# Kernel optimization log

Measured on AMD Instinct MI355X. Metric: run time of the kernel, lower is better.

## Reference

```python
import jax, jax.numpy as jnp
import numpy as np

D = 128        # dim
S = 64         # seq_len
NSYM = 128     # symbols
STACK = 16     # stack_size
DEPTH = 8      # max_depth (ACT recursion)
THRESH = 0.99  # act_threshold
EPS = 1e-6
RES = 0.1      # residual_weight
LAM_E = 0.01   # lambda_energy
TEMP = 1.0
B = 512


def _clin(xr, xi, Wr, Wi):
    # ComplexLinear: (Wr + i Wi)(xr + i xi)
    return xr @ Wr.T - xi @ Wi.T, xr @ Wi.T + xi @ Wr.T


def _cattn(zr, zi, wr, wi):
    # ComplexAttention: complex QKV projections, real softmax over concat(real,imag)
    qr, qi = _clin(zr, zi, wr[0], wi[0])
    kr, ki = _clin(zr, zi, wr[1], wi[1])
    vr, vi = _clin(zr, zi, wr[2], wi[2])
    qf = jnp.concatenate([qr, qi], -1)
    kf = jnp.concatenate([kr, ki], -1)
    a = jax.nn.softmax(jnp.einsum('bsd,btd->bst', qf, kf) * (D ** -0.5), axis=-1)
    return jnp.einsum('bst,btd->bsd', a, vr), jnp.einsum('bst,btd->bsd', a, vi)


def setup_inputs() -> dict:
    key = jax.random.key(0)
    ks = jax.random.split(key, 12)
    sc = 1.0 / np.sqrt(D)
    return {
        'z_real': jax.random.normal(ks[0], (B, S, D), jnp.float32),
        'z_imag': jax.random.normal(ks[1], (B, S, D), jnp.float32),
        'attn_wr': jax.random.normal(ks[2], (3, D, D), jnp.float32) * sc,
        'attn_wi': jax.random.normal(ks[3], (3, D, D), jnp.float32) * sc,
        'mem_wr': jax.random.normal(ks[4], (3, D, D), jnp.float32) * sc,
        'mem_wi': jax.random.normal(ks[5], (3, D, D), jnp.float32) * sc,
        'ctrl_w': jax.random.normal(ks[6], (2 * D, 3), jnp.float32) * sc,
        'ctrl_b': jnp.zeros((3,), jnp.float32),
        'halt_w': jax.random.normal(ks[7], (2 * D, 1), jnp.float32) * sc,
        'halt_b': jnp.zeros((1,), jnp.float32),
        'codebook': jax.random.normal(ks[8], (NSYM, 2 * D), jnp.float32) * 0.2,
        'adjacency': jax.random.normal(ks[9], (NSYM, NSYM), jnp.float32),
    }


def reference(z_real, z_imag, attn_wr, attn_wi, mem_wr, mem_wi,
              ctrl_w, ctrl_b, halt_w, halt_b, codebook, adjacency):
    b = z_real.shape[0]
    mem0 = jnp.zeros((b, STACK, 2 * D), z_real.dtype)
    ptr0 = jnp.zeros((b, STACK), z_real.dtype).at[:, 0].set(1.0)
    probs0 = jnp.zeros((b, NSYM), z_real.dtype)
    halt0 = jnp.zeros((b,), z_real.dtype)
    acc0 = jnp.zeros((b, S, 2 * D), z_real.dtype)

    def step(carry, t):
        zr, zi, mem, ptr, prev_probs, halt_acc, acc = carry
        # --- complex self-attention with residual recursion ---
        ar, ai = _cattn(zr, zi, attn_wr, attn_wi)
        zr = ar + RES * zr
        zi = ai + RES * zi
        # --- memory stack (push/pop/stay pointer machine) ---
        zf = jnp.concatenate([zr.mean(1), zi.mean(1)], -1)  # [B, 2D]
        g = jax.nn.sigmoid(zf @ ctrl_w + ctrl_b)
        tot = g.sum(-1, keepdims=True) + EPS
        push, pop, stay = g[:, 0:1] / tot, g[:, 1:2] / tot, g[:, 2:3] / tot
        ptr = push * jnp.roll(ptr, 1, axis=1) + pop * jnp.roll(ptr, -1, axis=1) + stay * ptr
        mem = mem * (1 - push[..., None]) + push[..., None] * zf[:, None, :]
        amr, ami = _cattn(mem[..., :D], mem[..., D:], mem_wr, mem_wi)
        read = (jnp.concatenate([amr, ami], -1) * ptr[..., None]).sum(1)  # [B, 2D]
        zr = zr + RES * read[:, None, :D]
        zi = zi + RES * read[:, None, D:]
        # --- grounded graph VQ: codebook distance + adjacency energy bias ---
        zf = jnp.concatenate([zr.mean(1), zi.mean(1)], -1)
        d = ((zf ** 2).sum(-1, keepdims=True) + (codebook ** 2).sum(-1)
             - 2 * zf @ codebook.T) / (2 * D)
        mag = jnp.sqrt(zr ** 2 + zi ** 2)
        up = jax.nn.softplus(mag.var() / (1.0 + EPS))  # complexity modulation
        gb = prev_probs @ adjacency
        d_tot = jnp.where(t == 0, d, d - LAM_E * up * jax.nn.sigmoid(gb))
        probs = jax.nn.softmax(-d_tot / TEMP, axis=-1)
        quant = probs @ codebook
        zr = zr + RES * quant[:, None, :D]
        zi = zi + RES * quant[:, None, D:]
        # --- ACT halting accumulation ---
        p = jax.nn.sigmoid(zf @ halt_w + halt_b)[:, 0]
        running = (halt_acc < THRESH).astype(zr.dtype)
        w = jnp.where(halt_acc + p * running >= THRESH, 1.0 - halt_acc, p) * running
        halt_acc = halt_acc + w
        acc = acc + w[:, None, None] * jnp.concatenate([zr, zi], -1)
        return (zr, zi, mem, ptr, probs, halt_acc, acc), None

    carry, _ = jax.lax.scan(step, (z_real, z_imag, mem0, ptr0, probs0, halt0, acc0),
                            jnp.arange(DEPTH))
    return carry[6]  # ACT-weighted state, [B, S, 2D]
```

## Files before the change

kernel.cpp:

```cpp
#include <hip/hip_runtime.h>
#include <math.h>

#define BB 512
#define SS 64
#define DD 128
#define FF 256
#define NSYM 128
#define STK 16
#define NDEPTH 8

typedef _Float16 half_t;
typedef __attribute__((ext_vector_type(4))) _Float16 half4;
typedef __attribute__((ext_vector_type(8))) _Float16 half8;
typedef __attribute__((ext_vector_type(4))) float f32x4;

#define Z_OFF      0ull
#define QKV_OFF    8388608ull
#define ZFW_OFF    33554432ull
#define QBUF_OFF   35651584ull
#define PTR_OFF    41943040ull
#define ZF1_OFF    41951232ull
#define ZF2_OFF    42082304ull
#define READ_OFF   42213376ull
#define PROBS_OFF  42344448ull
#define DELTA_OFF  42409984ull
#define HALT_OFF   42541056ull
#define PVAL_OFF   42541568ull
#define WACT_OFF   42542080ull
#define MAGP_OFF   42542592ull
#define MQKV_OFF   42740224ull
#define CB2_OFF    42936832ull

__global__ void k_buildwt32(const float* __restrict__ wr, const float* __restrict__ wi,
                            float* __restrict__ WT32) {
    int idx = blockIdx.x * 256 + threadIdx.x;
    if (idx >= 768 * 256) return;
    int col = idx >> 8;
    int e   = idx & 255;
    int h   = col >> 8;
    int c   = col & 255;
    const float* Wr = wr + h * DD * DD;
    const float* Wi = wi + h * DD * DD;
    float v;
    if (c < DD) {
        v = (e < DD) ? Wr[c * DD + e] : -Wi[c * DD + (e - DD)];
    } else {
        int j = c - DD;
        v = (e < DD) ? Wi[j * DD + e] : Wr[j * DD + (e - DD)];
    }
    WT32[idx] = v;
}

__global__ __launch_bounds__(256) void k_buildG(const float* __restrict__ WT32,
                                                half_t* __restrict__ GTh,
                                                half_t* __restrict__ GTl) {
    __shared__ float kcol[256];
    int n = blockIdx.x;
    int e = threadIdx.x;
    kcol[e] = WT32[65536 + e * 256 + n];
    __syncthreads();
    float s = 0.f;
    for (int c = 0; c < 256; ++c) s += kcol[c] * WT32[c * 256 + e];
    half_t h = (half_t)s;
    GTh[n * 256 + e] = h;
    GTl[n * 256 + e] = (half_t)(s - (float)h);
}

__global__ void k_splitWv(const float* __restrict__ WT32,
                          half_t* __restrict__ WvTh, half_t* __restrict__ WvTl) {
    int idx = blockIdx.x * 256 + threadIdx.x;
    float v = WT32[131072 + idx];
    half_t h = (half_t)v;
    WvTh[idx] = h;
    WvTl[idx] = (half_t)(v - (float)h);
}

__global__ void k_buildwt(const float* __restrict__ wr, const float* __restrict__ wi,
                          half_t* __restrict__ WTh, half_t* __restrict__ WTl) {
    int idx = blockIdx.x * 256 + threadIdx.x;
    if (idx >= 768 * 256) return;
    int col = idx >> 8;
    int e   = idx & 255;
    int h   = col >> 8;
    int c   = col & 255;
    const float* Wr = wr + h * DD * DD;
    const float* Wi = wi + h * DD * DD;
    float v;
    if (c < DD) {
        v = (e < DD) ? Wr[c * DD + e] : -Wi[c * DD + (e - DD)];
    } else {
        int j = c - DD;
        v = (e < DD) ? Wi[j * DD + e] : Wr[j * DD + (e - DD)];
    }
    half_t hh = (half_t)v;
    WTh[idx] = hh;
    WTl[idx] = (half_t)(v - (float)hh);
}

__global__ void k_cb2(const float* __restrict__ cb, float* __restrict__ cb2) {
    int n = threadIdx.x;
    float s = 0.f;
    for (int c = 0; c < FF; ++c) { float v = cb[n * FF + c]; s += v * v; }
    cb2[n] = s;
}

__global__ __launch_bounds__(256) void k_init(const float* __restrict__ zr_in,
                                              const float* __restrict__ zi_in,
                                              float* __restrict__ z, float* __restrict__ qbuf,
                                              float* __restrict__ ptrv,
                                              float* __restrict__ halt, float* __restrict__ acc,
                                              float* __restrict__ delta, float* __restrict__ wact) {
    size_t idx = (size_t)blockIdx.x * 256 + threadIdx.x;
    int c = (int)(idx & 255);
    size_t bs = idx >> 8;
    z[idx] = (c < DD) ? zr_in[bs * DD + c] : zi_in[bs * DD + (c - DD)];
    acc[idx] = 0.f;
    if (idx < 6291456) qbuf[idx] = 0.f;
    if (idx < 131072) delta[idx] = 0.f;
    if (idx < 8192)  ptrv[idx] = ((idx & 15) == 0) ? 1.f : 0.f;
    if (idx < 512)   { halt[idx] = 0.f; wact[idx] = 0.f; }
}

__global__ __launch_bounds__(512, 1) void k_attn8(
        float* __restrict__ z,
        const half_t* __restrict__ GTh, const half_t* __restrict__ GTl,
        const half_t* __restrict__ WvTh, const half_t* __restrict__ WvTl,
        const float* __restrict__ delta, const float* __restrict__ wact,
        float* __restrict__ acc, float* __restrict__ zf1g) {
    __shared__ half_t Zh[16896];
    __shared__ half_t Zl[16896];
    __shared__ half_t Ubuf[2][18432];
    __shared__ half_t Pbuf[2][4][1152];

    int b = blockIdx.x, tid = threadIdx.x;
    int w = tid >> 6, lane = tid & 63;
    int l15 = lane & 15, lq = lane >> 4;
    float* zb = z + (size_t)b * (SS * FF);
    float* accb = acc + (size_t)b * (SS * FF);

    float wa = wact[b];
    f32x4 dv = *(const f32x4*)(delta + b * FF + lane * 4);
    bool doacc = (wa != 0.0f);
#pragma unroll
    for (int it = 0; it < 8; ++it) {
        int i = w * 8 + it;
        f32x4 zv = *(const f32x4*)(zb + (size_t)i * FF + lane * 4);
        f32x4 x0;
#pragma unroll
        for (int jj = 0; jj < 4; ++jj) x0[jj] = zv[jj] + 0.1f * dv[jj];
        if (doacc) {
            f32x4 av = *(const f32x4*)(accb + (size_t)i * FF + lane * 4);
#pragma unroll
            for (int jj = 0; jj < 4; ++jj) av[jj] += wa * x0[jj];
            *(f32x4*)(accb + (size_t)i * FF + lane * 4) = av;
        }
        half4 h4, l4;
#pragma unroll
        for (int jj = 0; jj < 4; ++jj) {
            half_t h = (half_t)x0[jj];
            h4[jj] = h; l4[jj] = (half_t)(x0[jj] - (float)h);
        }
        *(half4*)&Zh[i * 264 + lane * 4] = h4;
        *(half4*)&Zl[i * 264 + lane * 4] = l4;
    }
    __syncthreads();

    {
        f32x4 tac[4][2];
#pragma unroll
        for (int mt = 0; mt < 4; ++mt)
#pragma unroll
            for (int nt = 0; nt < 2; ++nt) tac[mt][nt] = (f32x4){0.f, 0.f, 0.f, 0.f};
        __builtin_amdgcn_s_setprio(1);
#pragma unroll 2
        for (int kt = 0; kt < 8; ++kt) {
            int kc = kt * 32 + lq * 8;
            half8 ah[4], al[4], gh[2], gl[2];
#pragma unroll
            for (int mt = 0; mt < 4; ++mt) {
                int ro = (mt * 16 + l15) * 264 + kc;
                ah[mt] = *(const half8*)&Zh[ro];
                al[mt] = *(const half8*)&Zl[ro];
            }
#pragma unroll
            for (int nt = 0; nt < 2; ++nt) {
                size_t go = (size_t)(w * 32 + nt * 16 + l15) * 256 + kc;
                gh[nt] = *(const half8*)(GTh + go);
                gl[nt] = *(const half8*)(GTl + go);
            }
#pragma unroll
            for (int mt = 0; mt < 4; ++mt)
#pragma unroll
                for (int nt = 0; nt < 2; ++nt) {
                    tac[mt][nt] = __builtin_amdgcn_mfma_f32_16x16x32_f16(ah[mt], gh[nt], tac[mt][nt], 0, 0, 0);
                    tac[mt][nt] = __builtin_amdgcn_mfma_f32_16x16x32_f16(ah[mt], gl[nt], tac[mt][nt], 0, 0, 0);
                    tac[mt][nt] = __builtin_amdgcn_mfma_f32_16x16x32_f16(al[mt], gh[nt], tac[mt][nt], 0, 0, 0);
                }
        }
        __builtin_amdgcn_s_setprio(0);
        const float scale = 0.08838834764831845f;
#pragma unroll
        for (int mt = 0; mt < 4; ++mt)
#pragma unroll
            for (int nt = 0; nt < 2; ++nt)
#pragma unroll
                for (int r = 0; r < 4; ++r) {
                    int m = mt * 16 + lq * 4 + r;
                    int n = w * 32 + nt * 16 + l15;
                    float v = tac[mt][nt][r] * scale;
                    half_t h = (half_t)v;
                    Ubuf[0][m * 264 + n] = h;
                    Ubuf[1][m * 264 + n] = (half_t)(v - (float)h);
                }
    }
    __syncthreads();

    if (w < 4) {
        f32x4 sac[4];
#pragma unroll
        for (int jt = 0; jt < 4; ++jt) sac[jt] = (f32x4){0.f, 0.f, 0.f, 0.f};
        __builtin_amdgcn_s_setprio(1);
#pragma unroll 2
        for (int kt = 0; kt < 8; ++kt) {
            int kc = kt * 32 + lq * 8;
            int to = (w * 16 + l15) * 264 + kc;
            half8 bh = *(const half8*)&Ubuf[0][to];
            half8 bl = *(const half8*)&Ubuf[1][to];
            half8 ah[4], al[4];
#pragma unroll
            for (int jt = 0; jt < 4; ++jt) {
                int ro = (jt * 16 + l15) * 264 + kc;
                ah[jt] = *(const half8*)&Zh[ro];
                al[jt] = *(const half8*)&Zl[ro];
            }
#pragma unroll
            for (int jt = 0; jt < 4; ++jt) {
                sac[jt] = __builtin_amdgcn_mfma_f32_16x16x32_f16(ah[jt], bh, sac[jt], 0, 0, 0);
                sac[jt] = __builtin_amdgcn_mfma_f32_16x16x32_f16(ah[jt], bl, sac[jt], 0, 0, 0);
                sac[jt] = __builtin_amdgcn_mfma_f32_16x16x32_f16(al[jt], bh, sac[jt], 0, 0, 0);
            }
        }
        __builtin_amdgcn_s_setprio(0);
        float sv[4][4];
        float mx = -1e30f;
#pragma unroll
        for (int jt = 0; jt < 4; ++jt)
#pragma unroll
            for (int r = 0; r < 4; ++r) { sv[jt][r] = sac[jt][r]; mx = fmaxf(mx, sv[jt][r]); }
        mx = fmaxf(mx, __shfl_xor(mx, 16));
        mx = fmaxf(mx, __shfl_xor(mx, 32));
        float ssum = 0.f;
#pragma unroll
        for (int jt = 0; jt < 4; ++jt)
#pragma unroll
            for (int r = 0; r < 4; ++r) { float e = expf(sv[jt][r] - mx); sv[jt][r] = e; ssum += e; }
        ssum += __shfl_xor(ssum, 16);
        ssum += __shfl_xor(ssum, 32);
        float inv = 1.f / ssum;
#pragma unroll
        for (int jt = 0; jt < 4; ++jt) {
            half4 h4, l4;
#pragma unroll
            for (int r = 0; r < 4; ++r) {
                float pv = sv[jt][r] * inv;
                half_t hh = (half_t)pv;
                h4[r] = hh;
                l4[r] = (half_t)(pv - (float)hh);
            }
            *(half4*)&Pbuf[0][w][l15 * 72 + jt * 16 + lq * 4] = h4;
            *(half4*)&Pbuf[1][w][l15 * 72 + jt * 16 + lq * 4] = l4;
        }
    }

    f32x4 vac[4][2];
#pragma unroll
    for (int mt = 0; mt < 4; ++mt)
#pragma unroll
        for (int nt = 0; nt < 2; ++nt) vac[mt][nt] = (f32x4){0.f, 0.f, 0.f, 0.f};
    __builtin_amdgcn_s_setprio(1);
#pragma unroll 2
    for (int kt = 0; kt < 8; ++kt) {
        int kc = kt * 32 + lq * 8;
        half8 ah[4], al[4], gh[2], gl[2];
#pragma unroll
        for (int mt = 0; mt < 4; ++mt) {
            int ro = (mt * 16 + l15) * 264 + kc;
            ah[mt] = *(const half8*)&Zh[ro];
            al[mt] = *(const half8*)&Zl[ro];
        }
#pragma unroll
        for (int nt = 0; nt < 2; ++nt) {
            size_t go = (size_t)(w * 32 + nt * 16 + l15) * 256 + kc;
            gh[nt] = *(const half8*)(WvTh + go);
            gl[nt] = *(const half8*)(WvTl + go);
        }
#pragma unroll
        for (int mt = 0; mt < 4; ++mt)
#pragma unroll
            for (int nt = 0; nt < 2; ++nt) {
                vac[mt][nt] = __builtin_amdgcn_mfma_f32_16x16x32_f16(ah[mt], gh[nt], vac[mt][nt], 0, 0, 0);
                vac[mt][nt] = __builtin_amdgcn_mfma_f32_16x16x32_f16(ah[mt], gl[nt], vac[mt][nt], 0, 0, 0);
                vac[mt][nt] = __builtin_amdgcn_mfma_f32_16x16x32_f16(al[mt], gh[nt], vac[mt][nt], 0, 0, 0);
            }
    }
    __builtin_amdgcn_s_setprio(0);
    __syncthreads();

#pragma unroll
    for (int mt = 0; mt < 4; ++mt)
#pragma unroll
        for (int nt = 0; nt < 2; ++nt) {
            int n = w * 32 + nt * 16 + l15;
            int m0 = mt * 16 + lq * 4;
            half4 h4, l4;
#pragma unroll
            for (int r = 0; r < 4; ++r) {
                float v = vac[mt][nt][r];
                half_t h = (half_t)v;
                h4[r] = h; l4[r] = (half_t)(v - (float)h);
            }
            *(half4*)&Ubuf[0][n * 72 + m0] = h4;
            *(half4*)&Ubuf[1][n * 72 + m0] = l4;
        }
    __syncthreads();

    f32x4 oc[4][2];
#pragma unroll
    for (int mt = 0; mt < 4; ++mt)
#pragma unroll
        for (int nt = 0; nt < 2; ++nt) oc[mt][nt] = (f32x4){0.f, 0.f, 0.f, 0.f};
    __builtin_amdgcn_s_setprio(1);
#pragma unroll
    for (int kt = 0; kt < 2; ++kt) {
        half8 pah[4], pal[4];
#pragma unroll
        for (int mt = 0; mt < 4; ++mt) {
            int po = l15 * 72 + kt * 32 + lq * 8;
            pah[mt] = *(const half8*)&Pbuf[0][mt][po];
            pal[mt] = *(const half8*)&Pbuf[1][mt][po];
        }
#pragma unroll
        for (int nt = 0; nt < 2; ++nt) {
            int n = w * 32 + nt * 16 + l15;
            half8 vbh = *(const half8*)&Ubuf[0][n * 72 + kt * 32 + lq * 8];
            half8 vbl = *(const half8*)&Ubuf[1][n * 72 + kt * 32 + lq * 8];
#pragma unroll
            for (int mt = 0; mt < 4; ++mt) {
                oc[mt][nt] = __builtin_amdgcn_mfma_f32_16x16x32_f16(pah[mt], vbh, oc[mt][nt], 0, 0, 0);
                oc[mt][nt] = __builtin_amdgcn_mfma_f32_16x16x32_f16(pah[mt], vbl, oc[mt][nt], 0, 0, 0);
                oc[mt][nt] = __builtin_amdgcn_mfma_f32_16x16x32_f16(pal[mt], vbh, oc[mt][nt], 0, 0, 0);
            }
        }
    }
    __builtin_amdgcn_s_setprio(0);

    float zfs[2] = {0.f, 0.f};
#pragma unroll
    for (int mt = 0; mt < 4; ++mt)
#pragma unroll
        for (int nt = 0; nt < 2; ++nt)
#pragma unroll
            for (int r = 0; r < 4; ++r) {
                int i = mt * 16 + lq * 4 + r;
                int c = w * 32 + nt * 16 + l15;
                int zo = i * 264 + c;
                float x0 = (float)Zh[zo] + (float)Zl[zo];
                float z1 = oc[mt][nt][r] + 0.1f * x0;
                zb[(size_t)i * FF + c] = z1;
                zfs[nt] += z1;
            }
#pragma unroll
    for (int nt = 0; nt < 2; ++nt) {
        zfs[nt] += __shfl_xor(zfs[nt], 16);
        zfs[nt] += __shfl_xor(zfs[nt], 32);
    }
    if (lq == 0) {
#pragma unroll
        for (int nt = 0; nt < 2; ++nt)
            zf1g[b * FF + w * 32 + nt * 16 + l15] = zfs[nt] * (1.f / 64.f);
    }
}

__global__ __launch_bounds__(256) void gemm_split(const float* __restrict__ A,
                                                  const half_t* __restrict__ WTh,
                                                  const half_t* __restrict__ WTl,
                                                  float* __restrict__ C) {
    __shared__ float As[128][36];
    int bm = blockIdx.x / 6;
    int bn = blockIdx.x % 6;
    int tid = threadIdx.x;
    int w = tid >> 6;
    int lane = tid & 63;
    int wr = w >> 1, wc = w & 1;
    int l15 = lane & 15;
    int lq  = lane >> 4;

    f32x4 acc[4][4];
#pragma unroll
    for (int i = 0; i < 4; ++i)
#pragma unroll
        for (int j = 0; j < 4; ++j) acc[i][j] = (f32x4){0.f, 0.f, 0.f, 0.f};

    const float* Ablk = A + (size_t)bm * 128 * 256;
    int colbase = bn * 128 + wc * 64;

    int srow = tid >> 1;
    int sseg = (tid & 1) * 16;

    for (int k0 = 0; k0 < 256; k0 += 32) {
        __syncthreads();
        {
            const float* src = Ablk + (size_t)srow * 256 + k0 + sseg;
            f32x4 v0 = *(const f32x4*)(src);
            f32x4 v1 = *(const f32x4*)(src + 4);
            f32x4 v2 = *(const f32x4*)(src + 8);
            f32x4 v3 = *(const f32x4*)(src + 12);
            *(f32x4*)&As[srow][sseg]      = v0;
            *(f32x4*)&As[srow][sseg + 4]  = v1;
            *(f32x4*)&As[srow][sseg + 8]  = v2;
            *(f32x4*)&As[srow][sseg + 12] = v3;
        }
        __syncthreads();

        half8 bh[4], bl[4];
#pragma unroll
        for (int tj = 0; tj < 4; ++tj) {
            size_t off = (size_t)(colbase + tj * 16 + l15) * 256 + k0 + lq * 8;
            bh[tj] = *(const half8*)(WTh + off);
            bl[tj] = *(const half8*)(WTl + off);
        }

        half8 ah[4], al[4];
#pragma unroll
        for (int ti = 0; ti < 4; ++ti) {
            const float* ap = &As[wr * 64 + ti * 16 + l15][lq * 8];
            f32x4 a0 = *(const f32x4*)(ap);
            f32x4 a1 = *(const f32x4*)(ap + 4);
#pragma unroll
            for (int j = 0; j < 4; ++j) {
                float x = a0[j];
                half_t h = (half_t)x;
                ah[ti][j] = h;
                al[ti][j] = (half_t)(x - (float)h);
            }
#pragma unroll
            for (int j = 0; j < 4; ++j) {
                float x = a1[j];
                half_t h = (half_t)x;
                ah[ti][4 + j] = h;
                al[ti][4 + j] = (half_t)(x - (float)h);
            }
        }

#pragma unroll
        for (int ti = 0; ti < 4; ++ti)
#pragma unroll
            for (int tj = 0; tj < 4; ++tj)
                acc[ti][tj] = __builtin_amdgcn_mfma_f32_16x16x32_f16(ah[ti], bh[tj], acc[ti][tj], 0, 0, 0);
#pragma unroll
        for (int ti = 0; ti < 4; ++ti)
#pragma unroll
            for (int tj = 0; tj < 4; ++tj)
                acc[ti][tj] = __builtin_amdgcn_mfma_f32_16x16x32_f16(ah[ti], bl[tj], acc[ti][tj], 0, 0, 0);
#pragma unroll
        for (int ti = 0; ti < 4; ++ti)
#pragma unroll
            for (int tj = 0; tj < 4; ++tj)
                acc[ti][tj] = __builtin_amdgcn_mfma_f32_16x16x32_f16(al[ti], bh[tj], acc[ti][tj], 0, 0, 0);
    }

    float* Cb = C + (size_t)(bm * 128 + wr * 64) * 768 + bn * 128 + wc * 64;
#pragma unroll
    for (int ti = 0; ti < 4; ++ti)
#pragma unroll
        for (int tj = 0; tj < 4; ++tj) {
            int r0 = ti * 16 + lq * 4;
            int c0 = tj * 16 + l15;
#pragma unroll
            for (int r = 0; r < 4; ++r)
                Cb[(size_t)(r0 + r) * 768 + c0] = acc[ti][tj][r];
        }
}

__global__ __launch_bounds__(256, 2) void k_stack2(
        const float* __restrict__ zf1,
        const float* __restrict__ ctrl_w, const float* __restrict__ ctrl_b,
        float* __restrict__ ptrv, float* __restrict__ qbuf,
        const float* __restrict__ zfW,
        float* __restrict__ readv, float* __restrict__ zf2,
        const float* __restrict__ halt_w, const float* __restrict__ halt_b,
        float* __restrict__ pval,
        const float* __restrict__ z, float* __restrict__ magpart) {
    __shared__ float zf[256];
    __shared__ float g[3];
    __shared__ float oldp[16], np[16];
    __shared__ float Q[16][780];
    __shared__ float sm[16][17];
    __shared__ float rowmax[16], rowsum[16], pw[16];
    __shared__ float rd[256];
    __shared__ float red[256];

    int b = blockIdx.x, tid = threadIdx.x;
    int w = tid >> 6, lane = tid & 63;

    zf[tid] = zf1[b * FF + tid];
    if (tid < 16) oldp[tid] = ptrv[b * STK + tid];
    __syncthreads();
    if (w < 3) {
        float s = 0.f;
#pragma unroll
        for (int q = 0; q < 4; ++q) {
            int c = lane + 64 * q;
            s += zf[c] * ctrl_w[c * 3 + w];
        }
#pragma unroll
        for (int off = 1; off < 64; off <<= 1) s += __shfl_xor(s, off);
        if (lane == 0) g[w] = 1.f / (1.f + expf(-(s + ctrl_b[w])));
    }
    __syncthreads();
    float tot = g[0] + g[1] + g[2] + 1e-6f;
    float push = g[0] / tot, pop = g[1] / tot, stay = g[2] / tot;
    if (tid < 16) {
        float v = push * oldp[(tid + 15) & 15] + pop * oldp[(tid + 1) & 15] + stay * oldp[tid];
        np[tid] = v;
        ptrv[b * STK + tid] = v;
    }

    float omp = 1.f - push;
    float zw0 = push * zfW[b * 768 + tid];
    float zw1 = push * zfW[b * 768 + 256 + tid];
    float zw2 = push * zfW[b * 768 + 512 + tid];
    float* qb = qbuf + (size_t)b * (STK * 768);
#pragma unroll 4
    for (int t16 = 0; t16 < 16; ++t16) {
        float q0 = qb[t16 * 768 + tid]       * omp + zw0;
        float q1 = qb[t16 * 768 + 256 + tid] * omp + zw1;
        float q2 = qb[t16 * 768 + 512 + tid] * omp + zw2;
        qb[t16 * 768 + tid]       = q0;
        qb[t16 * 768 + 256 + tid] = q1;
        qb[t16 * 768 + 512 + tid] = q2;
        Q[t16][tid] = q0;
        Q[t16][256 + tid] = q1;
        Q[t16][512 + tid] = q2;
    }
    __syncthreads();

    {
        int i = tid >> 4, j = tid & 15;
        float s = 0.f;
#pragma unroll 4
        for (int c = 0; c < 256; c += 4) {
            f32x4 qi = *(const f32x4*)&Q[i][c];
            f32x4 kj = *(const f32x4*)&Q[j][256 + c];
            s += qi[0] * kj[0] + qi[1] * kj[1] + qi[2] * kj[2] + qi[3] * kj[3];
        }
        s *= 0.08838834764831845f;
        sm[i][j] = s;
        __syncthreads();
        if (tid < 16) {
            float m = -1e30f;
            for (int jj = 0; jj < 16; ++jj) m = fmaxf(m, sm[tid][jj]);
            float su = 0.f;
            for (int jj = 0; jj < 16; ++jj) su += expf(sm[tid][jj] - m);
            rowmax[tid] = m; rowsum[tid] = su;
        }
        __syncthreads();
        float p = expf(s - rowmax[i]) / rowsum[i];
        sm[i][j] = p;
        __syncthreads();
        if (tid < 16) {
            float a = 0.f;
            for (int s2 = 0; s2 < 16; ++s2) a += np[s2] * sm[s2][tid];
            pw[tid] = a;
        }
        __syncthreads();
    }

    {
        float a = 0.f;
#pragma unroll
        for (int jj = 0; jj < 16; ++jj) a += pw[jj] * Q[jj][512 + tid];
        rd[tid] = a;
        readv[b * FF + tid] = a;
        float z2 = zf[tid] + 0.1f * a;
        zf2[b * FF + tid] = z2;
        red[tid] = z2 * halt_w[tid];
        __syncthreads();
        for (int off = 128; off > 0; off >>= 1) {
            if (tid < off) red[tid] += red[tid + off];
            __syncthreads();
        }
        if (tid == 0) pval[b] = 1.f / (1.f + expf(-(red[0] + halt_b[0])));
        __syncthreads();
    }

    {
        int d = tid & 127, hf = tid >> 7;
        float rr = 0.1f * rd[d];
        float ri = 0.1f * rd[DD + d];
        const float* zb = z + (size_t)b * (SS * FF);
        float ms = 0.f, msq = 0.f;
        for (int s32 = 0; s32 < 32; ++s32) {
            int s = hf * 32 + s32;
            float zr = zb[s * FF + d] + rr;
            float zi = zb[s * FF + DD + d] + ri;
            float m2 = zr * zr + zi * zi;
            ms += sqrtf(m2); msq += m2;
        }
        red[tid] = ms;
        __syncthreads();
        for (int off = 128; off > 0; off >>= 1) {
            if (tid < off) red[tid] += red[tid + off];
            __syncthreads();
        }
        float tms = red[0];
        __syncthreads();
        red[tid] = msq;
        __syncthreads();
        for (int off = 128; off > 0; off >>= 1) {
            if (tid < off) red[tid] += red[tid + off];
            __syncthreads();
        }
        if (tid == 0) { magpart[2 * b] = tms; magpart[2 * b + 1] = red[0]; }
    }
}

__global__ __launch_bounds__(256) void k_vq2(
        const float* __restrict__ zf2g, const float* __restrict__ readv,
        float* __restrict__ probs, float* __restrict__ halt,
        const float* __restrict__ pvalg, const float* __restrict__ magp,
        const float* __restrict__ cb, const float* __restrict__ cb2,
        const float* __restrict__ adj,
        float* __restrict__ delta, float* __restrict__ wact, int t) {
    __shared__ float zf[256];
    __shared__ float pr[128];
    __shared__ float upred[8];
    __shared__ float zzred[4];
    __shared__ float mxred[4];
    __shared__ float sered[4];

    int b = blockIdx.x, tid = threadIdx.x;
    int w = tid >> 6, lane = tid & 63;

    zf[tid] = zf2g[b * FF + tid];

    float up = 0.f;
    if (t > 0) {
        f32x4 mv = *(const f32x4*)(magp + tid * 4);
        float pa = mv[0] + mv[2];
        float pb = mv[1] + mv[3];
#pragma unroll
        for (int off = 1; off < 64; off <<= 1) {
            pa += __shfl_xor(pa, off);
            pb += __shfl_xor(pb, off);
        }
        if (lane == 0) { upred[w * 2] = pa; upred[w * 2 + 1] = pb; }
    }
    __syncthreads();
    if (t > 0) {
        float tms  = upred[0] + upred[2] + upred[4] + upred[6];
        float tmsq = upred[1] + upred[3] + upred[5] + upred[7];
        const float N = 4194304.f;
        float mean = tms / N;
        float var = tmsq / N - mean * mean;
        float x = var / (1.f + 1e-6f);
        up = (x > 20.f) ? x : log1pf(expf(x));
    }

    {
        float part = zf[tid] * zf[tid];
#pragma unroll
        for (int off = 1; off < 64; off <<= 1) part += __shfl_xor(part, off);
        if (lane == 0) zzred[w] = part;
    }
    __syncthreads();
    float zz = zzred[0] + zzred[1] + zzred[2] + zzred[3];

    int n = tid >> 1, half = tid & 1;
    float dacc = 0.f;
    {
        const float* cbn = cb + n * FF + half * 128;
        const float* zfp = zf + half * 128;
#pragma unroll 8
        for (int c2 = 0; c2 < 128; c2 += 4) {
            f32x4 cv = *(const f32x4*)(cbn + c2);
            dacc += cv[0] * zfp[c2] + cv[1] * zfp[c2 + 1] + cv[2] * zfp[c2 + 2] + cv[3] * zfp[c2 + 3];
        }
        dacc += __shfl_xor(dacc, 1);
    }
    float gacc = 0.f;
    if (t > 0) {
        const float* pp = probs + b * NSYM;
        for (int k = half * 64; k < half * 64 + 64; ++k)
            gacc += pp[k] * adj[k * NSYM + n];
        gacc += __shfl_xor(gacc, 1);
    }

    float dist = (zz + cb2[n] - 2.f * dacc) * (1.f / 256.f);
    float dtot = dist;
    if (t > 0) dtot = dist - 0.01f * up * (1.f / (1.f + expf(-gacc)));
    float vval = -dtot;

    {
        float m = vval;
#pragma unroll
        for (int off = 1; off < 64; off <<= 1) m = fmaxf(m, __shfl_xor(m, off));
        if (lane == 0) mxred[w] = m;
    }
    __syncthreads();
    float mx = fmaxf(fmaxf(mxred[0], mxred[1]), fmaxf(mxred[2], mxred[3]));

    float e = expf(vval - mx);
    {
        float s = (half == 0) ? e : 0.f;
#pragma unroll
        for (int off = 1; off < 64; off <<= 1) s += __shfl_xor(s, off);
        if (lane == 0) sered[w] = s;
    }
    __syncthreads();
    float se = sered[0] + sered[1] + sered[2] + sered[3];
    float psm = e / se;
    if (half == 0) {
        pr[n] = psm;
        probs[b * NSYM + n] = psm;
    }
    __syncthreads();

    float q = 0.f;
#pragma unroll 4
    for (int k = 0; k < NSYM; ++k) q += pr[k] * cb[k * FF + tid];
    delta[b * FF + tid] = readv[b * FF + tid] + q;

    if (tid == 0) {
        float h = halt[b], p = pvalg[b];
        float running = (h < 0.99f) ? 1.f : 0.f;
        float w2 = (((h + p * running) >= 0.99f) ? (1.f - h) : p) * running;
        halt[b] = h + w2;
        wact[b] = w2;
    }
}

__global__ __launch_bounds__(256) void k_epilogue(const float* __restrict__ z,
                                                  const float* __restrict__ delta,
                                                  const float* __restrict__ wact,
                                                  float* __restrict__ acc) {
    int idx = blockIdx.x * 256 + threadIdx.x;
    int b = idx >> 14;
    int c = idx & 255;
    float wa = wact[b];
    if (wa != 0.0f)
        acc[idx] += wa * (z[idx] + 0.1f * delta[b * FF + c]);
}

extern "C" void kernel_launch(void* const* d_in, const int* in_sizes, int n_in,
                              void* d_out, int out_size, void* d_ws, size_t ws_size,
                              hipStream_t stream) {
    const float* z_real  = (const float*)d_in[0];
    const float* z_imag  = (const float*)d_in[1];
    const float* attn_wr = (const float*)d_in[2];
    const float* attn_wi = (const float*)d_in[3];
    const float* mem_wr  = (const float*)d_in[4];
    const float* mem_wi  = (const float*)d_in[5];
    const float* ctrl_w  = (const float*)d_in[6];
    const float* ctrl_b  = (const float*)d_in[7];
    const float* halt_w  = (const float*)d_in[8];
    const float* halt_b  = (const float*)d_in[9];
    const float* codebook  = (const float*)d_in[10];
    const float* adjacency = (const float*)d_in[11];

    float* ws = (float*)d_ws;
    float* z      = ws + Z_OFF;
    float* WT32   = ws + QKV_OFF;
    half_t* GTh   = (half_t*)(ws + QKV_OFF + 196608);
    half_t* GTl   = GTh + 65536;
    half_t* WvTh  = GTl + 65536;
    half_t* WvTl  = WvTh + 65536;
    float* zfW    = ws + ZFW_OFF;
    float* qbuf   = ws + QBUF_OFF;
    float* ptrv   = ws + PTR_OFF;
    float* zf1    = ws + ZF1_OFF;
    float* zf2    = ws + ZF2_OFF;
    float* readv  = ws + READ_OFF;
    float* probs  = ws + PROBS_OFF;
    float* delta  = ws + DELTA_OFF;
    float* halt   = ws + HALT_OFF;
    float* pval   = ws + PVAL_OFF;
    float* wact   = ws + WACT_OFF;
    float* magp   = ws + MAGP_OFF;
    half_t* MTh   = (half_t*)(ws + MQKV_OFF);
    half_t* MTl   = (half_t*)(ws + MQKV_OFF) + 196608;
    float* cb2    = ws + CB2_OFF;
    float* acc    = (float*)d_out;

    k_buildwt32<<<768, 256, 0, stream>>>(attn_wr, attn_wi, WT32);
    k_buildG<<<256, 256, 0, stream>>>(WT32, GTh, GTl);
    k_splitWv<<<256, 256, 0, stream>>>(WT32, WvTh, WvTl);
    k_buildwt<<<768, 256, 0, stream>>>(mem_wr, mem_wi, MTh, MTl);
    k_cb2<<<1, 128, 0, stream>>>(codebook, cb2);
    k_init<<<32768, 256, 0, stream>>>(z_real, z_imag, z, qbuf, ptrv, halt, acc,
                                      delta, wact);

    for (int t = 0; t < NDEPTH; ++t) {
        k_attn8<<<BB, 512, 0, stream>>>(z, GTh, GTl, WvTh, WvTl, delta, wact, acc, zf1);
        gemm_split<<<(BB / 128) * 6, 256, 0, stream>>>(zf1, MTh, MTl, zfW);
        k_stack2<<<BB, 256, 0, stream>>>(zf1, ctrl_w, ctrl_b, ptrv, qbuf, zfW,
                                         readv, zf2, halt_w, halt_b, pval, z, magp);
        k_vq2<<<BB, 256, 0, stream>>>(zf2, readv, probs, halt, pval, magp,
                                      codebook, cb2, adjacency, delta, wact, t);
    }
    k_epilogue<<<32768, 256, 0, stream>>>(z, delta, wact, acc);
}
```

Baseline: 917.5 us.

## Collapse stack memory attention into rank-one value state and pointer mass scalar

Replaces the per-batch 16-slot Q/K/V stack and its attention and softmax with a single running value vector plus a scalar pointer-mass sigma. This relies on every stack slot being updated identically, so the attention weights sum to the pointer mass and the read reduces to sigma times the shared value. Only the V projection GEMM is kept (2 of 6 column tiles), and the large qbuf read/write traffic and shared-memory softmax go away. Correctness depends on the identical-slot invariant holding, which is true given zero initialisation.

New measurement: 838.0 us. -8.7%, faster.

```diff
diff --git a/kernel.cpp b/kernel.cpp
--- a/kernel.cpp
+++ b/kernel.cpp
@@ -17,8 +17,8 @@
 #define Z_OFF      0ull
 #define QKV_OFF    8388608ull
 #define ZFW_OFF    33554432ull
-#define QBUF_OFF   35651584ull
-#define PTR_OFF    41943040ull
+#define MV_OFF     35651584ull
+#define SIG_OFF    35782656ull
 #define ZF1_OFF    41951232ull
 #define ZF2_OFF    42082304ull
 #define READ_OFF   42213376ull
@@ -75,28 +75,6 @@
     WvTl[idx] = (half_t)(v - (float)h);
 }
 
-__global__ void k_buildwt(const float* __restrict__ wr, const float* __restrict__ wi,
-                          half_t* __restrict__ WTh, half_t* __restrict__ WTl) {
-    int idx = blockIdx.x * 256 + threadIdx.x;
-    if (idx >= 768 * 256) return;
-    int col = idx >> 8;
-    int e   = idx & 255;
-    int h   = col >> 8;
-    int c   = col & 255;
-    const float* Wr = wr + h * DD * DD;
-    const float* Wi = wi + h * DD * DD;
-    float v;
-    if (c < DD) {
-        v = (e < DD) ? Wr[c * DD + e] : -Wi[c * DD + (e - DD)];
-    } else {
-        int j = c - DD;
-        v = (e < DD) ? Wi[j * DD + e] : Wr[j * DD + (e - DD)];
-    }
-    half_t hh = (half_t)v;
-    WTh[idx] = hh;
-    WTl[idx] = (half_t)(v - (float)hh);
-}
-
 __global__ void k_cb2(const float* __restrict__ cb, float* __restrict__ cb2) {
     int n = threadIdx.x;
     float s = 0.f;
@@ -106,8 +84,8 @@
 
 __global__ __launch_bounds__(256) void k_init(const float* __restrict__ zr_in,
                                               const float* __restrict__ zi_in,
-                                              float* __restrict__ z, float* __restrict__ qbuf,
-                                              float* __restrict__ ptrv,
+                                              float* __restrict__ z, float* __restrict__ mv,
+                                              float* __restrict__ sigma,
                                               float* __restrict__ halt, float* __restrict__ acc,
                                               float* __restrict__ delta, float* __restrict__ wact) {
     size_t idx = (size_t)blockIdx.x * 256 + threadIdx.x;
@@ -115,10 +93,8 @@
     size_t bs = idx >> 8;
     z[idx] = (c < DD) ? zr_in[bs * DD + c] : zi_in[bs * DD + (c - DD)];
     acc[idx] = 0.f;
-    if (idx < 6291456) qbuf[idx] = 0.f;
-    if (idx < 131072) delta[idx] = 0.f;
-    if (idx < 8192)  ptrv[idx] = ((idx & 15) == 0) ? 1.f : 0.f;
-    if (idx < 512)   { halt[idx] = 0.f; wact[idx] = 0.f; }
+    if (idx < 131072) { mv[idx] = 0.f; delta[idx] = 0.f; }
+    if (idx < 512)   { halt[idx] = 0.f; wact[idx] = 0.f; sigma[idx] = 1.f; }
 }
 
 __global__ __launch_bounds__(512, 1) void k_attn8(
@@ -381,13 +357,13 @@
     }
 }
 
-__global__ __launch_bounds__(256) void gemm_split(const float* __restrict__ A,
-                                                  const half_t* __restrict__ WTh,
-                                                  const half_t* __restrict__ WTl,
-                                                  float* __restrict__ C) {
+__global__ __launch_bounds__(256) void gemm_v(const float* __restrict__ A,
+                                              const half_t* __restrict__ WTh,
+                                              const half_t* __restrict__ WTl,
+                                              float* __restrict__ C) {
     __shared__ float As[128][36];
-    int bm = blockIdx.x / 6;
-    int bn = blockIdx.x % 6;
+    int bm = blockIdx.x >> 1;
+    int bn = blockIdx.x & 1;
     int tid = threadIdx.x;
     int w = tid >> 6;
     int lane = tid & 63;
@@ -469,7 +445,7 @@
                 acc[ti][tj] = __builtin_amdgcn_mfma_f32_16x16x32_f16(al[ti], bh[tj], acc[ti][tj], 0, 0, 0);
     }
 
-    float* Cb = C + (size_t)(bm * 128 + wr * 64) * 768 + bn * 128 + wc * 64;
+    float* Cb = C + (size_t)(bm * 128 + wr * 64) * 256 + bn * 128 + wc * 64;
 #pragma unroll
     for (int ti = 0; ti < 4; ++ti)
 #pragma unroll
@@ -478,25 +454,21 @@
             int c0 = tj * 16 + l15;
 #pragma unroll
             for (int r = 0; r < 4; ++r)
-                Cb[(size_t)(r0 + r) * 768 + c0] = acc[ti][tj][r];
-        }
-}
-
-__global__ __launch_bounds__(256, 2) void k_stack2(
+                Cb[(size_t)(r0 + r) * 256 + c0] = acc[ti][tj][r];
+        }
+}
+
+__global__ __launch_bounds__(256) void k_stack3(
         const float* __restrict__ zf1,
         const float* __restrict__ ctrl_w, const float* __restrict__ ctrl_b,
-        float* __restrict__ ptrv, float* __restrict__ qbuf,
-        const float* __restrict__ zfW,
+        float* __restrict__ sigma, float* __restrict__ mv,
+        const float* __restrict__ zfWv,
         float* __restrict__ readv, float* __restrict__ zf2,
         const float* __restrict__ halt_w, const float* __restrict__ halt_b,
         float* __restrict__ pval,
         const float* __restrict__ z, float* __restrict__ magpart) {
     __shared__ float zf[256];
     __shared__ float g[3];
-    __shared__ float oldp[16], np[16];
-    __shared__ float Q[16][780];
-    __shared__ float sm[16][17];
-    __shared__ float rowmax[16], rowsum[16], pw[16];
     __shared__ float rd[256];
     __shared__ float red[256];
 
@@ -504,7 +476,6 @@
     int w = tid >> 6, lane = tid & 63;
 
     zf[tid] = zf1[b * FF + tid];
-    if (tid < 16) oldp[tid] = ptrv[b * STK + tid];
     __syncthreads();
     if (w < 3) {
         float s = 0.f;
@@ -520,79 +491,26 @@
     __syncthreads();
     float tot = g[0] + g[1] + g[2] + 1e-6f;
     float push = g[0] / tot, pop = g[1] / tot, stay = g[2] / tot;
-    if (tid < 16) {
-        float v = push * oldp[(tid + 15) & 15] + pop * oldp[(tid + 1) & 15] + stay * oldp[tid];
-        np[tid] = v;
-        ptrv[b * STK + tid] = v;
-    }
+    float signew = sigma[b] * (push + pop + stay);
+    if (tid == 0) sigma[b] = signew;
 
     float omp = 1.f - push;
-    float zw0 = push * zfW[b * 768 + tid];
-    float zw1 = push * zfW[b * 768 + 256 + tid];
-    float zw2 = push * zfW[b * 768 + 512 + tid];
-    float* qb = qbuf + (size_t)b * (STK * 768);
-#pragma unroll 4
-    for (int t16 = 0; t16 < 16; ++t16) {
-        float q0 = qb[t16 * 768 + tid]       * omp + zw0;
-        float q1 = qb[t16 * 768 + 256 + tid] * omp + zw1;
-        float q2 = qb[t16 * 768 + 512 + tid] * omp + zw2;
-        qb[t16 * 768 + tid]       = q0;
-        qb[t16 * 768 + 256 + tid] = q1;
-        qb[t16 * 768 + 512 + tid] = q2;
-        Q[t16][tid] = q0;
-        Q[t16][256 + tid] = q1;
-        Q[t16][512 + tid] = q2;
-    }
-    __syncthreads();
-
-    {
-        int i = tid >> 4, j = tid & 15;
-        float s = 0.f;
-#pragma unroll 4
-        for (int c = 0; c < 256; c += 4) {
-            f32x4 qi = *(const f32x4*)&Q[i][c];
-            f32x4 kj = *(const f32x4*)&Q[j][256 + c];
-            s += qi[0] * kj[0] + qi[1] * kj[1] + qi[2] * kj[2] + qi[3] * kj[3];
-        }
-        s *= 0.08838834764831845f;
-        sm[i][j] = s;
+    float m2v = mv[b * FF + tid] * omp + push * zfWv[b * FF + tid];
+    mv[b * FF + tid] = m2v;
+
+    float a = signew * m2v;
+    rd[tid] = a;
+    readv[b * FF + tid] = a;
+    float z2 = zf[tid] + 0.1f * a;
+    zf2[b * FF + tid] = z2;
+    red[tid] = z2 * halt_w[tid];
+    __syncthreads();
+    for (int off = 128; off > 0; off >>= 1) {
+        if (tid < off) red[tid] += red[tid + off];
         __syncthreads();
-        if (tid < 16) {
-            float m = -1e30f;
-            for (int jj = 0; jj < 16; ++jj) m = fmaxf(m, sm[tid][jj]);
-            float su = 0.f;
-            for (int jj = 0; jj < 16; ++jj) su += expf(sm[tid][jj] - m);
-            rowmax[tid] = m; rowsum[tid] = su;
-        }
-        __syncthreads();
-        float p = expf(s - rowmax[i]) / rowsum[i];
-        sm[i][j] = p;
-        __syncthreads();
-        if (tid < 16) {
-            float a = 0.f;
-            for (int s2 = 0; s2 < 16; ++s2) a += np[s2] * sm[s2][tid];
-            pw[tid] = a;
-        }
-        __syncthreads();
-    }
-
-    {
-        float a = 0.f;
-#pragma unroll
-        for (int jj = 0; jj < 16; ++jj) a += pw[jj] * Q[jj][512 + tid];
-        rd[tid] = a;
-        readv[b * FF + tid] = a;
-        float z2 = zf[tid] + 0.1f * a;
-        zf2[b * FF + tid] = z2;
-        red[tid] = z2 * halt_w[tid];
-        __syncthreads();
-        for (int off = 128; off > 0; off >>= 1) {
-            if (tid < off) red[tid] += red[tid + off];
-            __syncthreads();
-        }
-        if (tid == 0) pval[b] = 1.f / (1.f + expf(-(red[0] + halt_b[0])));
-        __syncthreads();
-    }
+    }
+    if (tid == 0) pval[b] = 1.f / (1.f + expf(-(red[0] + halt_b[0])));
+    __syncthreads();
 
     {
         int d = tid & 127, hf = tid >> 7;
@@ -646,9 +564,9 @@
 
     float up = 0.f;
     if (t > 0) {
-        f32x4 mv = *(const f32x4*)(magp + tid * 4);
-        float pa = mv[0] + mv[2];
-        float pb = mv[1] + mv[3];
+        f32x4 mv4 = *(const f32x4*)(magp + tid * 4);
+        float pa = mv4[0] + mv4[2];
+        float pb = mv4[1] + mv4[3];
 #pragma unroll
         for (int off = 1; off < 64; off <<= 1) {
             pa += __shfl_xor(pa, off);
@@ -775,9 +693,11 @@
     half_t* GTl   = GTh + 65536;
     half_t* WvTh  = GTl + 65536;
     half_t* WvTl  = WvTh + 65536;
-    float* zfW    = ws + ZFW_OFF;
-    float* qbuf   = ws + QBUF_OFF;
-    float* ptrv   = ws + PTR_OFF;
+    float* zfWv   = ws + ZFW_OFF;
+    half_t* MvTh  = (half_t*)(ws + ZFW_OFF + 131072);
+    half_t* MvTl  = MvTh + 65536;
+    float* mv     = ws + MV_OFF;
+    float* sigma  = ws + SIG_OFF;
     float* zf1    = ws + ZF1_OFF;
     float* zf2    = ws + ZF2_OFF;
     float* readv  = ws + READ_OFF;
@@ -787,23 +707,23 @@
     float* pval   = ws + PVAL_OFF;
     float* wact   = ws + WACT_OFF;
     float* magp   = ws + MAGP_OFF;
-    half_t* MTh   = (half_t*)(ws + MQKV_OFF);
-    half_t* MTl   = (half_t*)(ws + MQKV_OFF) + 196608;
+    float* MT32   = ws + MQKV_OFF;
     float* cb2    = ws + CB2_OFF;
     float* acc    = (float*)d_out;
 
     k_buildwt32<<<768, 256, 0, stream>>>(attn_wr, attn_wi, WT32);
     k_buildG<<<256, 256, 0, stream>>>(WT32, GTh, GTl);
     k_splitWv<<<256, 256, 0, stream>>>(WT32, WvTh, WvTl);
-    k_buildwt<<<768, 256, 0, stream>>>(mem_wr, mem_wi, MTh, MTl);
+    k_buildwt32<<<768, 256, 0, stream>>>(mem_wr, mem_wi, MT32);
+    k_splitWv<<<256, 256, 0, stream>>>(MT32, MvTh, MvTl);
     k_cb2<<<1, 128, 0, stream>>>(codebook, cb2);
-    k_init<<<32768, 256, 0, stream>>>(z_real, z_imag, z, qbuf, ptrv, halt, acc,
+    k_init<<<32768, 256, 0, stream>>>(z_real, z_imag, z, mv, sigma, halt, acc,
                                       delta, wact);
 
     for (int t = 0; t < NDEPTH; ++t) {
         k_attn8<<<BB, 512, 0, stream>>>(z, GTh, GTl, WvTh, WvTl, delta, wact, acc, zf1);
-        gemm_split<<<(BB / 128) * 6, 256, 0, stream>>>(zf1, MTh, MTl, zfW);
-        k_stack2<<<BB, 256, 0, stream>>>(zf1, ctrl_w, ctrl_b, ptrv, qbuf, zfW,
+        gemm_v<<<8, 256, 0, stream>>>(zf1, MvTh, MvTl, zfWv);
+        k_stack3<<<BB, 256, 0, stream>>>(zf1, ctrl_w, ctrl_b, sigma, mv, zfWv,
                                          readv, zf2, halt_w, halt_b, pval, z, magp);
         k_vq2<<<BB, 256, 0, stream>>>(zf2, readv, probs, halt, pval, magp,
                                       codebook, cb2, adjacency, delta, wact, t);
```
